# Performance work log

Hardware: AMD Instinct MI355X
Metric: run time of the kernel (lower is better)

## Reference

```python
import jax, jax.numpy as jnp
import numpy as np

D_MODEL, N_HEADS, D_STATE, N_GROUPS, CHUNK = 2048, 32, 64, 1, 256
BATCH, SEQLEN = 2, 4096


def setup_inputs() -> dict:
    key = jax.random.key(0)
    ks = jax.random.split(key, 8)
    s = 0.02
    d, h, n, g = D_MODEL, N_HEADS, D_STATE, N_GROUPS
    return {
        "x": jax.random.normal(ks[0], (BATCH, SEQLEN, d), jnp.float32),
        "A_log": jnp.log(jnp.arange(1, h + 1, dtype=jnp.float32)),
        "D": jnp.ones((h,), jnp.float32),
        "B_w": jax.random.normal(ks[1], (g * n, d), jnp.float32) * s,
        "B_b": jnp.zeros((g * n,), jnp.float32),
        "C_w": jax.random.normal(ks[2], (g * n, d), jnp.float32) * s,
        "C_b": jnp.zeros((g * n,), jnp.float32),
        "dt_w": jax.random.normal(ks[3], (h, d), jnp.float32) * s,
        "dt_b": jnp.zeros((h,), jnp.float32),
        "out_w": jax.random.normal(ks[4], (d, d), jnp.float32) * s,
        "out_b": jnp.zeros((d,), jnp.float32),
    }


def segsum(v):
    # v: [..., T] -> [..., T, T]; out[i,j] = sum_{k=j+1..i} v[k] for i>=j, -inf else
    cs = jnp.cumsum(v, axis=-1)
    seg = cs[..., :, None] - cs[..., None, :]
    T = v.shape[-1]
    mask = jnp.tril(jnp.ones((T, T), bool))
    return jnp.where(mask, seg, -jnp.inf)


def _ssd(x, A_log, D, B_w, B_b, C_w, C_b, dt_w, dt_b, out_w, out_b):
    b, t, d = x.shape
    h = A_log.shape[0]
    n = B_w.shape[0] // N_GROUPS
    p = d // h
    l = CHUNK
    c = t // l

    A = -jnp.exp(A_log.astype(jnp.float32))                      # [h]
    B = (x @ B_w.T + B_b).reshape(b, t, N_GROUPS, n)             # g=1
    C = (x @ C_w.T + C_b).reshape(b, t, N_GROUPS, n)
    B = jnp.broadcast_to(B, (b, t, h, n))                        # repeat groups -> heads
    C = jnp.broadcast_to(C, (b, t, h, n))
    dt = jax.nn.softplus(x @ dt_w.T + dt_b)                      # [b,t,h]
    xh = x.reshape(b, t, h, p)

    # chunked SSD (Mamba2 mamba_chunk_scan_combined math)
    xc = xh.reshape(b, c, l, h, p)
    Bc = B.reshape(b, c, l, h, n)
    Cc = C.reshape(b, c, l, h, n)
    dtc = dt.reshape(b, c, l, h)
    dA = jnp.transpose(dtc * A, (0, 3, 1, 2))                    # [b,h,c,l]
    A_cumsum = jnp.cumsum(dA, axis=-1)                           # [b,h,c,l]

    # 1. intra-chunk (diagonal blocks)
    L = jnp.exp(segsum(dA))                                      # [b,h,c,l,l]
    xdt = xc * dtc[..., None]                                    # [b,c,l,h,p]
    Y_diag = jnp.einsum('bclhn,bcshn,bhcls,bcshp->bclhp', Cc, Bc, L, xdt)

    # 2. per-chunk final states
    decay_states = jnp.exp(A_cumsum[..., -1:] - A_cumsum)        # [b,h,c,l]
    states = jnp.einsum('bclhn,bhcl,bclhp->bchpn', Bc, decay_states, xdt)

    # 3. inter-chunk recurrence on chunk states
    states = jnp.concatenate([jnp.zeros_like(states[:, :1]), states], axis=1)  # [b,c+1,h,p,n]
    dA_last = jnp.pad(A_cumsum[..., -1], ((0, 0), (0, 0), (1, 0)))             # [b,h,c+1]
    decay_chunk = jnp.exp(segsum(dA_last))                                     # [b,h,c+1,c+1]
    new_states = jnp.einsum('bhzc,bchpn->bzhpn', decay_chunk, states)
    prev_states = new_states[:, :-1]                                           # [b,c,h,p,n]

    # 4. state -> output contribution
    state_decay_out = jnp.exp(A_cumsum)                          # [b,h,c,l]
    Y_off = jnp.einsum('bclhn,bchpn,bhcl->bclhp', Cc, prev_states, state_decay_out)

    Y = (Y_diag + Y_off).reshape(b, t, h, p) + D[None, None, :, None] * xh
    return Y.reshape(b, t, d) @ out_w.T + out_b


def reference(x, A_log, D, B_w, B_b, C_w, C_b, dt_w, dt_b, out_w, out_b):
    return _ssd(x, A_log, D, B_w, B_b, C_w, C_b, dt_w, dt_b, out_w, out_b)
```

## Files before the change

kernel.cpp:

```cpp
#include <hip/hip_runtime.h>
#include <hip/hip_bf16.h>
#include <math.h>

namespace {
constexpr int kDModel = 2048;
constexpr int kHeads  = 32;
constexpr int kState  = 64;
constexpr int kP      = 64;
constexpr int kChunk  = 256;
constexpr int kNChunk = 16;
constexpr int kBatch  = 2;
constexpr int kSeq    = 4096;
constexpr int kM      = kBatch * kSeq;
}

typedef __bf16 bf16_t;
typedef __attribute__((ext_vector_type(8))) __bf16 bf16x8;
typedef __attribute__((ext_vector_type(4))) __bf16 bf16x4;
typedef __attribute__((ext_vector_type(4))) float f32x4;

__device__ __forceinline__ void gload_lds16(const void* g, void* l) {
    __builtin_amdgcn_global_load_lds(
        (const __attribute__((address_space(1))) void*)g,
        (__attribute__((address_space(3))) void*)l,
        16, 0, 0);
}

template <int MODE>
__global__ __launch_bounds__(256)
void gemm_mfma(const bf16_t* __restrict__ A, const bf16_t* __restrict__ W,
               int K, int N,
               const float* __restrict__ b0, const float* __restrict__ b1,
               const float* __restrict__ b2,
               float* __restrict__ o0f, bf16_t* __restrict__ o0h,
               bf16_t* __restrict__ o1h, float* __restrict__ o2f)
{
    __shared__ __bf16 AstS[128 * 32];
    __shared__ __bf16 WstS[128 * 32];
    const int tid  = threadIdx.x;
    const int lane = tid & 63;
    const int wave = tid >> 6;
    const int wm = (wave >> 1) * 64;
    const int wn = (wave & 1) * 64;
    const int l15 = lane & 15, quad = lane >> 4;
    const int m0 = blockIdx.y * 128;
    const int n0 = blockIdx.x * 128;
    const int u0 = tid, u1 = tid + 256;

    f32x4 acc[4][4];
    #pragma unroll
    for (int i = 0; i < 4; ++i)
        #pragma unroll
        for (int j = 0; j < 4; ++j)
            acc[i][j] = (f32x4){0.f, 0.f, 0.f, 0.f};

    for (int k0 = 0; k0 < K; k0 += 32) {
        gload_lds16(A + (size_t)(m0 + (u0 >> 2)) * K + k0 + (u0 & 3) * 8, AstS + u0 * 8);
        gload_lds16(A + (size_t)(m0 + (u1 >> 2)) * K + k0 + (u1 & 3) * 8, AstS + u1 * 8);
        gload_lds16(W + (size_t)(n0 + (u0 >> 2)) * K + k0 + (u0 & 3) * 8, WstS + u0 * 8);
        gload_lds16(W + (size_t)(n0 + (u1 >> 2)) * K + k0 + (u1 & 3) * 8, WstS + u1 * 8);
        __syncthreads();
        bf16x8 af[4], bfr[4];
        #pragma unroll
        for (int mi = 0; mi < 4; ++mi)
            af[mi] = *reinterpret_cast<const bf16x8*>(&AstS[(wm + mi * 16 + l15) * 32 + quad * 8]);
        #pragma unroll
        for (int ni = 0; ni < 4; ++ni)
            bfr[ni] = *reinterpret_cast<const bf16x8*>(&WstS[(wn + ni * 16 + l15) * 32 + quad * 8]);
        #pragma unroll
        for (int mi = 0; mi < 4; ++mi)
            #pragma unroll
            for (int ni = 0; ni < 4; ++ni)
                acc[mi][ni] = __builtin_amdgcn_mfma_f32_16x16x32_bf16(
                    af[mi], bfr[ni], acc[mi][ni], 0, 0, 0);
        __syncthreads();
    }

    #pragma unroll
    for (int mi = 0; mi < 4; ++mi) {
        #pragma unroll
        for (int reg = 0; reg < 4; ++reg) {
            const int r = m0 + wm + mi * 16 + quad * 4 + reg;
            #pragma unroll
            for (int ni = 0; ni < 4; ++ni) {
                const float v = acc[mi][ni][reg];
                if (MODE == 0) {
                    const int c = n0 + wn + ni * 16 + l15;
                    o0f[(size_t)r * N + c] = v + b0[c];
                } else {
                    const int n = n0 + wn + ni * 16 + l15;
                    if (n < 64) {
                        o0h[(size_t)r * 64 + n] = (bf16_t)(v + b0[n]);
                    } else if (n < 128) {
                        o1h[(size_t)r * 64 + (n - 64)] = (bf16_t)(v + b1[n - 64]);
                    } else if (n < 160) {
                        float z = v + b2[n - 128];
                        o2f[(size_t)r * 32 + (n - 128)] = (z > 20.f) ? z : log1pf(expf(z));
                    }
                }
            }
        }
    }
}

__global__ __launch_bounds__(256)
void cvt_bf16_kernel(const float* __restrict__ src, bf16_t* __restrict__ dst, int n)
{
    const int i = (blockIdx.x * 256 + threadIdx.x) * 4;
    if (i + 3 < n) {
        const float4 v = *reinterpret_cast<const float4*>(src + i);
        dst[i + 0] = (bf16_t)v.x;
        dst[i + 1] = (bf16_t)v.y;
        dst[i + 2] = (bf16_t)v.z;
        dst[i + 3] = (bf16_t)v.w;
    }
}

__global__ __launch_bounds__(256)
void pack_w_kernel(const float* __restrict__ B_w, const float* __restrict__ C_w,
                   const float* __restrict__ dt_w, bf16_t* __restrict__ wcat)
{
    const int idx = blockIdx.x * 256 + threadIdx.x;
    const int r = idx >> 11, k = idx & 2047;
    float v = 0.f;
    if (r < 64)       v = B_w[r * 2048 + k];
    else if (r < 128) v = C_w[(r - 64) * 2048 + k];
    else if (r < 160) v = dt_w[(r - 128) * 2048 + k];
    wcat[idx] = (bf16_t)v;
}

__global__ __launch_bounds__(kChunk)
void dtcumsum_kernel(const float* __restrict__ dtm, const float* __restrict__ A_log,
                     float* __restrict__ Acs)
{
    const int blk = blockIdx.x;
    const int ci = blk & (kNChunk - 1);
    const int hi = (blk >> 4) & (kHeads - 1);
    const int bi = blk >> 9;
    const int t = threadIdx.x;
    const float Ah = -expf(A_log[hi]);
    __shared__ float s[kChunk];
    s[t] = dtm[((size_t)bi * kSeq + ci * kChunk + t) * kHeads + hi] * Ah;
    __syncthreads();
    for (int off = 1; off < kChunk; off <<= 1) {
        const float add = (t >= off) ? s[t - off] : 0.f;
        __syncthreads();
        s[t] += add;
        __syncthreads();
    }
    Acs[((size_t)(bi * kHeads + hi) * kNChunk + ci) * kChunk + t] = s[t];
}

__global__ __launch_bounds__(256)
void bT_kernel(const bf16_t* __restrict__ Bb16, bf16_t* __restrict__ bTg)
{
    const int ci = blockIdx.x & (kNChunk - 1);
    const int bi = blockIdx.x >> 4;
    const size_t rowbase = (size_t)bi * kSeq + ci * kChunk;
    __shared__ __bf16 T[64 * 264];
    const int tid = threadIdx.x;
    bf16x8 v[8];
    #pragma unroll
    for (int e = 0; e < 8; ++e)
        v[e] = *reinterpret_cast<const bf16x8*>(Bb16 + (rowbase + tid) * 64 + e * 8);
    #pragma unroll
    for (int e = 0; e < 8; ++e)
        #pragma unroll
        for (int j = 0; j < 8; ++j)
            T[(e * 8 + j) * 264 + tid] = v[e][j];
    __syncthreads();
    const int n = tid >> 2, seg = (tid & 3) * 64;
    bf16_t* dst = bTg + ((size_t)(bi * kNChunk + ci)) * (64 * 256) + n * 256 + seg;
    #pragma unroll
    for (int j = 0; j < 8; ++j) {
        *reinterpret_cast<bf16x8*>(dst + j * 8) =
            *reinterpret_cast<const bf16x8*>(&T[n * 264 + seg + j * 8]);
    }
}

__global__ __launch_bounds__(256)
void xdtT_kernel(const bf16_t* __restrict__ xb, const float* __restrict__ dtm,
                 bf16_t* __restrict__ xdtT)
{
    const int blk = blockIdx.x;
    const int hi = blk & (kHeads - 1);
    const int ci = (blk >> 5) & (kNChunk - 1);
    const int bi = blk >> 9;
    const size_t rowbase = (size_t)bi * kSeq + ci * kChunk;
    __shared__ __bf16 T[64 * 264];
    const int tid = threadIdx.x;
    const float d = dtm[(rowbase + tid) * kHeads + hi];
    bf16x8 v[8];
    #pragma unroll
    for (int e = 0; e < 8; ++e)
        v[e] = *reinterpret_cast<const bf16x8*>(xb + (rowbase + tid) * kDModel + hi * kP + e * 8);
    #pragma unroll
    for (int e = 0; e < 8; ++e)
        #pragma unroll
        for (int j = 0; j < 8; ++j)
            T[(e * 8 + j) * 264 + tid] = (__bf16)((float)v[e][j] * d);
    __syncthreads();
    const int p = tid >> 2, seg = (tid & 3) * 64;
    bf16_t* dst = xdtT + (size_t)blk * (64 * 256) + p * 256 + seg;
    #pragma unroll
    for (int j = 0; j < 8; ++j) {
        *reinterpret_cast<bf16x8*>(dst + j * 8) =
            *reinterpret_cast<const bf16x8*>(&T[p * 264 + seg + j * 8]);
    }
}

__global__ __launch_bounds__(256)
void states_mfma(const bf16_t* __restrict__ xdtT, const bf16_t* __restrict__ bTg,
                 const float* __restrict__ Acs, float* __restrict__ states)
{
    const int blk = blockIdx.x;
    const int hi = blk & (kHeads - 1);
    const int ci = (blk >> 5) & (kNChunk - 1);
    const int bi = blk >> 9;
    __shared__ __bf16 Xa[64 * 264];
    __shared__ __bf16 Bt[64 * 264];
    __shared__ float dec[kChunk];
    const int tid = threadIdx.x;
    const int lane = tid & 63;
    const int wave = tid >> 6;
    const int l15 = lane & 15, quad = lane >> 4;

    const float* acs = Acs + ((size_t)(bi * kHeads + hi) * kNChunk + ci) * kChunk;
    dec[tid] = expf(acs[kChunk - 1] - acs[tid]);
    __syncthreads();

    const bf16_t* bsrc = bTg + ((size_t)(bi * kNChunk + ci)) * (64 * 256);
    const bf16_t* xsrc = xdtT + (size_t)blk * (64 * 256);
    #pragma unroll
    for (int e = 0; e < 8; ++e) {
        const int u = e * 256 + tid;
        const int r = u >> 5, seg = (u & 31) * 8;
        *reinterpret_cast<bf16x8*>(&Bt[r * 264 + seg]) =
            *reinterpret_cast<const bf16x8*>(bsrc + r * 256 + seg);
        bf16x8 xv = *reinterpret_cast<const bf16x8*>(xsrc + r * 256 + seg);
        bf16x8 xo;
        #pragma unroll
        for (int j = 0; j < 8; ++j)
            xo[j] = (__bf16)((float)xv[j] * dec[seg + j]);
        *reinterpret_cast<bf16x8*>(&Xa[r * 264 + seg]) = xo;
    }
    __syncthreads();

    f32x4 acc[4];
    #pragma unroll
    for (int ni = 0; ni < 4; ++ni) acc[ni] = (f32x4){0.f, 0.f, 0.f, 0.f};
    #pragma unroll
    for (int kk = 0; kk < 8; ++kk) {
        const bf16x8 af = *reinterpret_cast<const bf16x8*>(
            &Xa[(wave * 16 + l15) * 264 + kk * 32 + quad * 8]);
        #pragma unroll
        for (int ni = 0; ni < 4; ++ni) {
            const bf16x8 bf = *reinterpret_cast<const bf16x8*>(
                &Bt[(ni * 16 + l15) * 264 + kk * 32 + quad * 8]);
            acc[ni] = __builtin_amdgcn_mfma_f32_16x16x32_bf16(af, bf, acc[ni], 0, 0, 0);
        }
    }
    float* sp = states + (size_t)blk * (kP * kState);
    #pragma unroll
    for (int reg = 0; reg < 4; ++reg) {
        const int p = wave * 16 + quad * 4 + reg;
        #pragma unroll
        for (int ni = 0; ni < 4; ++ni)
            sp[(size_t)p * kState + ni * 16 + l15] = acc[ni][reg];
    }
}

__global__ __launch_bounds__(256)
void chunkscan_kernel(const float* __restrict__ states, const float* __restrict__ Acs,
                      float* __restrict__ prevs)
{
    const int hi = blockIdx.x & (kHeads - 1);
    const int bi = blockIdx.x >> 5;
    const int tid = threadIdx.x;
    __shared__ float ea[kNChunk];
    if (tid < kNChunk)
        ea[tid] = expf(Acs[((size_t)(bi * kHeads + hi) * kNChunk + tid) * kChunk + kChunk - 1]);
    __syncthreads();
    float P[16];
    {
        float* pp = prevs + ((size_t)(bi * kNChunk + 0) * kHeads + hi) * (kP * kState);
        #pragma unroll
        for (int e = 0; e < 16; ++e) { P[e] = 0.f; pp[e * 256 + tid] = 0.f; }
    }
    for (int c = 1; c < kNChunk; ++c) {
        const float* sp = states + ((size_t)(bi * kNChunk + (c - 1)) * kHeads + hi) * (kP * kState);
        float* pp = prevs + ((size_t)(bi * kNChunk + c) * kHeads + hi) * (kP * kState);
        const float e_ = ea[c - 1];
        #pragma unroll
        for (int e = 0; e < 16; ++e) {
            P[e] = fmaf(e_, P[e], sp[e * 256 + tid]);
            pp[e * 256 + tid] = P[e];
        }
    }
}

__global__ __launch_bounds__(256)
void ychunk_mfma(const float* __restrict__ x, const bf16_t* __restrict__ Bb16,
                 const bf16_t* __restrict__ Cb16, const bf16_t* __restrict__ xdtT,
                 const float* __restrict__ Acs, const float* __restrict__ prevs,
                 const float* __restrict__ Dvec, bf16_t* __restrict__ Y)
{
    const int blk = blockIdx.x;
    const int lt = blk & 3;
    const int hi = (blk >> 2) & (kHeads - 1);
    const int ci = (blk >> 7) & (kNChunk - 1);
    const int bi = blk >> 11;
    __shared__ float acs_s[kChunk];
    __shared__ __bf16 Cs[64 * 72];
    __shared__ __bf16 Bs[64 * 72];
    __shared__ __bf16 Xt[64 * 72];
    __shared__ __bf16 Sp[64 * 72];
    const int tid = threadIdx.x;
    const int lane = tid & 63;
    const int wave = tid >> 6;
    const int l15 = lane & 15, quad = lane >> 4;
    const size_t rowbase = (size_t)bi * kSeq + ci * kChunk;
    const bf16_t* xdsrc = xdtT + ((size_t)((bi * kNChunk + ci) * kHeads + hi)) * (64 * 256);

    acs_s[tid] = Acs[((size_t)(bi * kHeads + hi) * kNChunk + ci) * kChunk + tid];
    #pragma unroll
    for (int e = 0; e < 2; ++e) {
        const int u = e * 256 + tid;
        const int r = u >> 3, seg = (u & 7) * 8;
        *reinterpret_cast<bf16x8*>(&Cs[r * 72 + seg]) =
            *reinterpret_cast<const bf16x8*>(Cb16 + (rowbase + lt * 64 + r) * 64 + seg);
    }
    const float* pp = prevs + ((size_t)(bi * kNChunk + ci) * kHeads + hi) * (kP * kState);
    #pragma unroll
    for (int e = 0; e < 4; ++e) {
        const int idx = e * 1024 + tid * 4;
        const int r = idx >> 6, c = idx & 63;
        const float4 vp = *reinterpret_cast<const float4*>(pp + idx);
        bf16x4 p4;
        p4[0] = (__bf16)vp.x; p4[1] = (__bf16)vp.y;
        p4[2] = (__bf16)vp.z; p4[3] = (__bf16)vp.w;
        *reinterpret_cast<bf16x4*>(&Bs[r * 72 + c]) = p4;
    }
    __syncthreads();

    bf16x8 af[2];
    af[0] = *reinterpret_cast<const bf16x8*>(&Cs[(wave * 16 + l15) * 72 + quad * 8]);
    af[1] = *reinterpret_cast<const bf16x8*>(&Cs[(wave * 16 + l15) * 72 + 32 + quad * 8]);

    f32x4 yacc[4];
    #pragma unroll
    for (int ni = 0; ni < 4; ++ni) yacc[ni] = (f32x4){0.f, 0.f, 0.f, 0.f};
    #pragma unroll
    for (int ni = 0; ni < 4; ++ni) {
        const bf16x8 b0 = *reinterpret_cast<const bf16x8*>(&Bs[(ni * 16 + l15) * 72 + quad * 8]);
        const bf16x8 b1 = *reinterpret_cast<const bf16x8*>(&Bs[(ni * 16 + l15) * 72 + 32 + quad * 8]);
        yacc[ni] = __builtin_amdgcn_mfma_f32_16x16x32_bf16(af[0], b0, yacc[ni], 0, 0, 0);
        yacc[ni] = __builtin_amdgcn_mfma_f32_16x16x32_bf16(af[1], b1, yacc[ni], 0, 0, 0);
    }
    const int mrow = wave * 16 + quad * 4;
    {
        float es[4];
        #pragma unroll
        for (int reg = 0; reg < 4; ++reg) es[reg] = expf(acs_s[lt * 64 + mrow + reg]);
        #pragma unroll
        for (int ni = 0; ni < 4; ++ni)
            #pragma unroll
            for (int reg = 0; reg < 4; ++reg) yacc[ni][reg] *= es[reg];
    }

    for (int st = 0; st <= lt; ++st) {
        __syncthreads();
        #pragma unroll
        for (int e = 0; e < 2; ++e) {
            const int u = e * 256 + tid;
            const int r = u >> 3, seg = (u & 7) * 8;
            *reinterpret_cast<bf16x8*>(&Bs[r * 72 + seg]) =
                *reinterpret_cast<const bf16x8*>(Bb16 + (rowbase + st * 64 + r) * 64 + seg);
            *reinterpret_cast<bf16x8*>(&Xt[r * 72 + seg]) =
                *reinterpret_cast<const bf16x8*>(xdsrc + r * 256 + st * 64 + seg);
        }
        __syncthreads();
        f32x4 sacc[4];
        #pragma unroll
        for (int ni = 0; ni < 4; ++ni) sacc[ni] = (f32x4){0.f, 0.f, 0.f, 0.f};
        #pragma unroll
        for (int ni = 0; ni < 4; ++ni) {
            const bf16x8 b0 = *reinterpret_cast<const bf16x8*>(&Bs[(ni * 16 + l15) * 72 + quad * 8]);
            const bf16x8 b1 = *reinterpret_cast<const bf16x8*>(&Bs[(ni * 16 + l15) * 72 + 32 + quad * 8]);
            sacc[ni] = __builtin_amdgcn_mfma_f32_16x16x32_bf16(af[0], b0, sacc[ni], 0, 0, 0);
            sacc[ni] = __builtin_amdgcn_mfma_f32_16x16x32_bf16(af[1], b1, sacc[ni], 0, 0, 0);
        }
        #pragma unroll
        for (int reg = 0; reg < 4; ++reg) {
            const int l = lt * 64 + mrow + reg;
            const float al = acs_s[l];
            #pragma unroll
            for (int ni = 0; ni < 4; ++ni) {
                const int scol = ni * 16 + l15;
                const int sg = st * 64 + scol;
                float v = sacc[ni][reg] * expf(al - acs_s[sg]);
                if (st == lt && sg > l) v = 0.f;
                Sp[(mrow + reg) * 72 + scol] = (__bf16)v;
            }
        }
        __syncthreads();
        const bf16x8 as0 = *reinterpret_cast<const bf16x8*>(&Sp[(wave * 16 + l15) * 72 + quad * 8]);
        const bf16x8 as1 = *reinterpret_cast<const bf16x8*>(&Sp[(wave * 16 + l15) * 72 + 32 + quad * 8]);
        #pragma unroll
        for (int ni = 0; ni < 4; ++ni) {
            const bf16x8 x0 = *reinterpret_cast<const bf16x8*>(&Xt[(ni * 16 + l15) * 72 + quad * 8]);
            const bf16x8 x1 = *reinterpret_cast<const bf16x8*>(&Xt[(ni * 16 + l15) * 72 + 32 + quad * 8]);
            yacc[ni] = __builtin_amdgcn_mfma_f32_16x16x32_bf16(as0, x0, yacc[ni], 0, 0, 0);
            yacc[ni] = __builtin_amdgcn_mfma_f32_16x16x32_bf16(as1, x1, yacc[ni], 0, 0, 0);
        }
    }

    const float Dh = Dvec[hi];
    #pragma unroll
    for (int reg = 0; reg < 4; ++reg) {
        const size_t tg = rowbase + lt * 64 + mrow + reg;
        #pragma unroll
        for (int ni = 0; ni < 4; ++ni) {
            const int p = ni * 16 + l15;
            const float v = yacc[ni][reg] + Dh * x[tg * kDModel + hi * kP + p];
            Y[tg * kDModel + hi * kP + p] = (bf16_t)v;
        }
    }
}

extern "C" void kernel_launch(void* const* d_in, const int* in_sizes, int n_in,
                              void* d_out, int out_size, void* d_ws, size_t ws_size,
                              hipStream_t stream)
{
    (void)in_sizes; (void)n_in; (void)out_size; (void)ws_size;
    const float* x     = (const float*)d_in[0];
    const float* A_log = (const float*)d_in[1];
    const float* Dvec  = (const float*)d_in[2];
    const float* B_w   = (const float*)d_in[3];
    const float* B_b   = (const float*)d_in[4];
    const float* C_w   = (const float*)d_in[5];
    const float* C_b   = (const float*)d_in[6];
    const float* dt_w  = (const float*)d_in[7];
    const float* dt_b  = (const float*)d_in[8];
    const float* out_w = (const float*)d_in[9];
    const float* out_b = (const float*)d_in[10];
    float* out = (float*)d_out;

    float* ws = (float*)d_ws;
    float* dtm    = ws;
    float* Acs    = dtm + (size_t)kM * kHeads;
    float* states = Acs + (size_t)kBatch * kHeads * kNChunk * kChunk;
    float* prevs  = states + (size_t)kBatch * kNChunk * kHeads * kP * kState;
    bf16_t* xb    = (bf16_t*)(prevs + (size_t)kBatch * kNChunk * kHeads * kP * kState);
    bf16_t* Y     = xb;
    bf16_t* Bb16  = xb + (size_t)kM * kDModel;
    bf16_t* Cb16  = Bb16 + (size_t)kM * kState;
    bf16_t* xdtT  = Cb16 + (size_t)kM * kState;
    bf16_t* bTg   = xdtT + (size_t)kM * kDModel;
    bf16_t* wcat  = bTg + (size_t)kBatch * kNChunk * kState * kChunk;
    bf16_t* wob   = wcat + (size_t)256 * kDModel;

    const dim3 blk(256);
    cvt_bf16_kernel<<<dim3(kM * kDModel / 1024), blk, 0, stream>>>(x, xb, kM * kDModel);
    cvt_bf16_kernel<<<dim3(kDModel * kDModel / 1024), blk, 0, stream>>>(out_w, wob, kDModel * kDModel);
    pack_w_kernel<<<dim3(256 * kDModel / 256), blk, 0, stream>>>(B_w, C_w, dt_w, wcat);
    gemm_mfma<1><<<dim3(2, kM / 128), blk, 0, stream>>>(xb, wcat, kDModel, 0,
                                                        B_b, C_b, dt_b,
                                                        nullptr, Bb16, Cb16, dtm);
    dtcumsum_kernel<<<dim3(kBatch * kHeads * kNChunk), dim3(kChunk), 0, stream>>>(dtm, A_log, Acs);
    bT_kernel<<<dim3(kBatch * kNChunk), blk, 0, stream>>>(Bb16, bTg);
    xdtT_kernel<<<dim3(kBatch * kNChunk * kHeads), blk, 0, stream>>>(xb, dtm, xdtT);
    states_mfma<<<dim3(kBatch * kNChunk * kHeads), blk, 0, stream>>>(xdtT, bTg, Acs, states);
    chunkscan_kernel<<<dim3(kBatch * kHeads), blk, 0, stream>>>(states, Acs, prevs);
    ychunk_mfma<<<dim3(kBatch * kNChunk * kHeads * 4), blk, 0, stream>>>(
        x, Bb16, Cb16, xdtT, Acs, prevs, Dvec, Y);
    gemm_mfma<0><<<dim3(kDModel / 128, kM / 128), blk, 0, stream>>>(Y, wob, kDModel, kDModel,
                                                                    out_b, nullptr, nullptr,
                                                                    out, nullptr, nullptr, nullptr);
}
```

Measured before the change: 418.6 us.

## Replace output projection GEMM with 256x256-tile triple-buffered kernel on K-packed layouts

Adds a dedicated output-projection GEMM that uses 256x256 tiles, 512 threads, a three-stage LDS pipeline fed by direct global-to-LDS loads, wave priority hints and a swizzled block order. ychunk now writes Y in a K-major packed layout of 8-element groups, and a new pack kernel converts out_w into the same layout, so tile loads are contiguous 16-byte transfers. This targets the final 8192x2048x2048 GEMM, the largest single cost. It raises register and LDS use per block and launches only 256 blocks, which may leave occupancy or load balance uneven.

```diff
diff --git a/kernel.cpp b/kernel.cpp
--- a/kernel.cpp
+++ b/kernel.cpp
@@ -103,6 +103,112 @@
     }
 }
 
+__global__ __launch_bounds__(512, 2)
+void gemm256_out(const bf16_t* __restrict__ Ap, const bf16_t* __restrict__ Bp,
+                 const float* __restrict__ bias, float* __restrict__ C)
+{
+    constexpr int M = 8192, N = 2048, NT = 2048 / 32;
+    __shared__ __bf16 Ab[3][4 * 256 * 8];
+    __shared__ __bf16 Bb[3][4 * 256 * 8];
+    const int tid  = threadIdx.x;
+    const int lane = tid & 63;
+    const int wave = tid >> 6;
+    const int l15 = lane & 15, quad = lane >> 4;
+    const int swz = ((blockIdx.x & 7) << 5) | (blockIdx.x >> 3);
+    const int m0 = (swz & 31) * 256;
+    const int n0 = (swz >> 5) * 256;
+    const int wm = (wave >> 2) * 128;
+    const int wn = (wave & 3) * 64;
+
+    const int u0 = tid, u1 = tid + 512;
+    auto stage = [&](int t2, int stb) {
+        const int ks0 = t2 * 4;
+        const bf16_t* As = Ap + ((size_t)ks0 * M + m0) * 8;
+        const bf16_t* Bs = Bp + ((size_t)ks0 * N + n0) * 8;
+        __bf16* Al = &Ab[stb][0];
+        __bf16* Bl = &Bb[stb][0];
+        gload_lds16(As + ((size_t)(u0 >> 8) * M + (u0 & 255)) * 8, Al + u0 * 8);
+        gload_lds16(As + ((size_t)(u1 >> 8) * M + (u1 & 255)) * 8, Al + u1 * 8);
+        gload_lds16(Bs + ((size_t)(u0 >> 8) * N + (u0 & 255)) * 8, Bl + u0 * 8);
+        gload_lds16(Bs + ((size_t)(u1 >> 8) * N + (u1 & 255)) * 8, Bl + u1 * 8);
+    };
+
+    f32x4 acc[8][4];
+    #pragma unroll
+    for (int i = 0; i < 8; ++i)
+        #pragma unroll
+        for (int j = 0; j < 4; ++j)
+            acc[i][j] = (f32x4){0.f, 0.f, 0.f, 0.f};
+
+    stage(0, 0);
+    stage(1, 1);
+    asm volatile("s_waitcnt vmcnt(4)" ::: "memory");
+    __builtin_amdgcn_s_barrier();
+
+    int cur = 0;
+    for (int t = 0; t < NT; ++t) {
+        const __bf16* Ac = &Ab[cur][0];
+        const __bf16* Bc = &Bb[cur][0];
+        int stb = cur + 2; if (stb >= 3) stb -= 3;
+
+        bf16x8 af[4], bfr[4];
+        #pragma unroll
+        for (int mi = 0; mi < 4; ++mi)
+            af[mi] = *reinterpret_cast<const bf16x8*>(
+                &Ac[(quad * 256 + wm + mi * 16 + l15) * 8]);
+        #pragma unroll
+        for (int nj = 0; nj < 4; ++nj)
+            bfr[nj] = *reinterpret_cast<const bf16x8*>(
+                &Bc[(quad * 256 + wn + nj * 16 + l15) * 8]);
+        if (t < NT - 2) stage(t + 2, stb);
+        __builtin_amdgcn_s_setprio(1);
+        #pragma unroll
+        for (int mi = 0; mi < 4; ++mi)
+            #pragma unroll
+            for (int nj = 0; nj < 4; ++nj)
+                acc[mi][nj] = __builtin_amdgcn_mfma_f32_16x16x32_bf16(
+                    af[mi], bfr[nj], acc[mi][nj], 0, 0, 0);
+        __builtin_amdgcn_s_setprio(0);
+
+        #pragma unroll
+        for (int mi = 0; mi < 4; ++mi)
+            af[mi] = *reinterpret_cast<const bf16x8*>(
+                &Ac[(quad * 256 + wm + 64 + mi * 16 + l15) * 8]);
+        __builtin_amdgcn_s_setprio(1);
+        #pragma unroll
+        for (int mi = 0; mi < 4; ++mi)
+            #pragma unroll
+            for (int nj = 0; nj < 4; ++nj)
+                acc[4 + mi][nj] = __builtin_amdgcn_mfma_f32_16x16x32_bf16(
+                    af[mi], bfr[nj], acc[4 + mi][nj], 0, 0, 0);
+        __builtin_amdgcn_s_setprio(0);
+
+        if (t < NT - 2) {
+            asm volatile("s_waitcnt vmcnt(4)" ::: "memory");
+        } else if (t < NT - 1) {
+            asm volatile("s_waitcnt vmcnt(0)" ::: "memory");
+        }
+        if (t < NT - 1) __builtin_amdgcn_s_barrier();
+        cur = cur + 1; if (cur == 3) cur = 0;
+    }
+
+    float bia[4];
+    #pragma unroll
+    for (int nj = 0; nj < 4; ++nj) bia[nj] = bias[n0 + wn + nj * 16 + l15];
+    #pragma unroll
+    for (int mi = 0; mi < 8; ++mi) {
+        #pragma unroll
+        for (int reg = 0; reg < 4; ++reg) {
+            const int r = m0 + wm + mi * 16 + quad * 4 + reg;
+            #pragma unroll
+            for (int nj = 0; nj < 4; ++nj) {
+                const int c = n0 + wn + nj * 16 + l15;
+                C[(size_t)r * N + c] = acc[mi][nj][reg] + bia[nj];
+            }
+        }
+    }
+}
+
 __global__ __launch_bounds__(256)
 void cvt_bf16_kernel(const float* __restrict__ src, bf16_t* __restrict__ dst, int n)
 {
@@ -114,6 +220,19 @@
         dst[i + 2] = (bf16_t)v.z;
         dst[i + 3] = (bf16_t)v.w;
     }
+}
+
+__global__ __launch_bounds__(256)
+void pack_wob_kernel(const float* __restrict__ W, bf16_t* __restrict__ Wp)
+{
+    const int idx = blockIdx.x * 256 + threadIdx.x;
+    const int n = idx >> 8, ks = idx & 255;
+    const float4 v0 = *reinterpret_cast<const float4*>(W + (size_t)n * 2048 + ks * 8);
+    const float4 v1 = *reinterpret_cast<const float4*>(W + (size_t)n * 2048 + ks * 8 + 4);
+    bf16x8 o;
+    o[0] = (__bf16)v0.x; o[1] = (__bf16)v0.y; o[2] = (__bf16)v0.z; o[3] = (__bf16)v0.w;
+    o[4] = (__bf16)v1.x; o[5] = (__bf16)v1.y; o[6] = (__bf16)v1.z; o[7] = (__bf16)v1.w;
+    *reinterpret_cast<bf16x8*>(Wp + ((size_t)ks * 2048 + n) * 8) = o;
 }
 
 __global__ __launch_bounds__(256)
@@ -303,7 +422,7 @@
 void ychunk_mfma(const float* __restrict__ x, const bf16_t* __restrict__ Bb16,
                  const bf16_t* __restrict__ Cb16, const bf16_t* __restrict__ xdtT,
                  const float* __restrict__ Acs, const float* __restrict__ prevs,
-                 const float* __restrict__ Dvec, bf16_t* __restrict__ Y)
+                 const float* __restrict__ Dvec, bf16_t* __restrict__ Yp)
 {
     const int blk = blockIdx.x;
     const int lt = blk & 3;
@@ -423,7 +542,7 @@
         for (int ni = 0; ni < 4; ++ni) {
             const int p = ni * 16 + l15;
             const float v = yacc[ni][reg] + Dh * x[tg * kDModel + hi * kP + p];
-            Y[tg * kDModel + hi * kP + p] = (bf16_t)v;
+            Yp[((size_t)(hi * 8 + (p >> 3)) * (size_t)kM + tg) * 8 + (p & 7)] = (bf16_t)v;
         }
     }
 }
@@ -462,7 +581,7 @@
 
     const dim3 blk(256);
     cvt_bf16_kernel<<<dim3(kM * kDModel / 1024), blk, 0, stream>>>(x, xb, kM * kDModel);
-    cvt_bf16_kernel<<<dim3(kDModel * kDModel / 1024), blk, 0, stream>>>(out_w, wob, kDModel * kDModel);
+    pack_wob_kernel<<<dim3(kDModel * 256 / 256), blk, 0, stream>>>(out_w, wob);
     pack_w_kernel<<<dim3(256 * kDModel / 256), blk, 0, stream>>>(B_w, C_w, dt_w, wcat);
     gemm_mfma<1><<<dim3(2, kM / 128), blk, 0, stream>>>(xb, wcat, kDModel, 0,
                                                         B_b, C_b, dt_b,
@@ -474,7 +593,5 @@
     chunkscan_kernel<<<dim3(kBatch * kHeads), blk, 0, stream>>>(states, Acs, prevs);
     ychunk_mfma<<<dim3(kBatch * kNChunk * kHeads * 4), blk, 0, stream>>>(
         x, Bb16, Cb16, xdtT, Acs, prevs, Dvec, Y);
-    gemm_mfma<0><<<dim3(kDModel / 128, kM / 128), blk, 0, stream>>>(Y, wob, kDModel, kDModel,
-                                                                    out_b, nullptr, nullptr,
-                                                                    out, nullptr, nullptr, nullptr);
-}
+    gemm256_out<<<dim3(256), dim3(512), 0, stream>>>(Y, wob, out_b, out);
+}
```

New measurement: 383.9 us. -8.3%, faster.
